# Kernel tuning notes

Hardware: AMD Instinct MI355X
Metric: run time of the kernel (lower is better)

## Reference

```python
import jax, jax.numpy as jnp
import numpy as np

B, H, T_STEPS = 256, 1024, 128


def setup_inputs() -> dict:
    key = jax.random.key(0)
    ks = jax.random.split(key, 17)
    s = 1.0 / np.sqrt(H)
    def W(k):
        return jax.random.uniform(k, (H, H), jnp.float32, -s, s)
    def b(k):
        return jax.random.uniform(k, (H,), jnp.float32, -s, s)
    names = ["Wif", "Wii", "Wio", "Wic", "Whf", "Whi", "Who", "Whc"]
    d = {}
    for i, n in enumerate(names):
        d[n] = W(ks[i])
        d["b" + n[1:]] = b(ks[8 + i])
    d["x_0"] = jax.random.normal(ks[16], (B, H), jnp.float32)
    d["T"] = T_STEPS
    return d


def reference(Wif, bif, Wii, bii, Wio, bio, Wic, bic,
              Whf, bhf, Whi, bhi, Who, bho, Whc, bhc, x_0, T):
    def step(carry, _):
        x, h, c = carry
        gf = jax.nn.sigmoid(h @ Whf.T + bhf + x @ Wif.T + bif)
        gi = jax.nn.sigmoid(h @ Whi.T + bhi + x @ Wii.T + bii)
        cp = jnp.tanh(h @ Whc.T + bhc + x @ Wic.T + bic)
        c = gf * c + gi * cp
        go = jax.nn.sigmoid(h @ Who.T + bho + x @ Wio.T + bio)
        h = go * jnp.tanh(c)
        return (h, h, c), h  # next x_input is hidden

    h0 = jnp.zeros((B, H), x_0.dtype)
    c0 = jnp.zeros((B, H), x_0.dtype)
    _, hs = jax.lax.scan(step, (x_0, h0, c0), None, length=T - 1)
    # trajectory[0] = x_0, trajectory[t+1] = hidden after step t  -> [T, B, H]
    return jnp.concatenate([x_0[None], hs], axis=0)
```

## Files before the change

### kernel.cpp

```cpp
#include <hip/hip_runtime.h>
#include <stdint.h>


#define BATCH 256
#define HID   1024

typedef __bf16 bf16_t;
typedef bf16_t bf16x8 __attribute__((ext_vector_type(8)));
typedef float  f32x16 __attribute__((ext_vector_type(16)));
typedef float  f32x4  __attribute__((ext_vector_type(4)));
typedef float  f32x2  __attribute__((ext_vector_type(2)));
typedef unsigned int u32;
typedef unsigned long long u64;

#define WC_OFF    (64ull << 20)
#define BIAS_OFF  (72ull << 20)
#define FLAG_OFF  ((72ull << 20) + (1ull << 16))

#define LDS_BYTES 131584

__device__ __forceinline__ void gload_lds16(const void* g, void* l) {
  auto gp = reinterpret_cast<const __attribute__((address_space(1))) unsigned int*>(
      reinterpret_cast<uintptr_t>(g));
  auto lp = reinterpret_cast<__attribute__((address_space(3))) unsigned int*>(
      reinterpret_cast<uintptr_t>(l));
  __builtin_amdgcn_global_load_lds(gp, lp, 16, 0, 0);
}

__global__ __launch_bounds__(256) void k_setup(
    const float* __restrict__ wf, const float* __restrict__ wi_,
    const float* __restrict__ wo, const float* __restrict__ wc,
    const float* __restrict__ hf, const float* __restrict__ hi,
    const float* __restrict__ ho, const float* __restrict__ hc,
    const float* __restrict__ bf_, const float* __restrict__ bi_,
    const float* __restrict__ bo_, const float* __restrict__ bc_,
    const float* __restrict__ hbf, const float* __restrict__ hbi,
    const float* __restrict__ hbo, const float* __restrict__ hbc,
    const float* __restrict__ x0, float* __restrict__ out,
    bf16_t* __restrict__ Wc, bf16_t* __restrict__ Wi, float* __restrict__ bias,
    bf16_t* __restrict__ hsh, u32* __restrict__ flags, int nflags)
{
  int bid = blockIdx.x;
  if (bid < 4096) {
    int r = bid, j = r >> 2, g = r & 3;
    const float *wip, *whp, *bip, *bhp;
    switch (g) {
      case 0:  wip = wf;  whp = hf; bip = bf_; bhp = hbf; break;
      case 1:  wip = wi_; whp = hi; bip = bi_; bhp = hbi; break;
      case 2:  wip = wo;  whp = ho; bip = bo_; bhp = hbo; break;
      default: wip = wc;  whp = hc; bip = bc_; bhp = hbc; break;
    }
    int k = threadIdx.x * 4;
    f32x4 a = *(const f32x4*)(wip + (size_t)j * HID + k);
    f32x4 b = *(const f32x4*)(whp + (size_t)j * HID + k);
    union { bf16_t h[4]; u64 v; } pc, pi;
#pragma unroll
    for (int t = 0; t < 4; ++t) { pc.h[t] = (bf16_t)(a[t] + b[t]); pi.h[t] = (bf16_t)a[t]; }
    *(u64*)(Wc + (size_t)r * HID + k) = pc.v;
    *(u64*)(Wi + (size_t)r * HID + k) = pi.v;
    if (threadIdx.x == 0) bias[r] = bip[j] + bhp[j];
  } else {
    int gid = (bid - 4096) * 256 + threadIdx.x;
    int i = gid * 4;
    f32x4 v = *(const f32x4*)(x0 + i);
    __builtin_nontemporal_store(v, (f32x4*)(out + i));
    union { bf16_t h[4]; u64 u; } p;
#pragma unroll
    for (int t = 0; t < 4; ++t) p.h[t] = (bf16_t)v[t];
    *(u64*)(hsh + i) = p.u;
    if (gid < nflags) flags[gid] = 0;
  }
}

__global__ __launch_bounds__(512, 2) void k_lstm(
    const bf16_t* __restrict__ Wc, const bf16_t* __restrict__ Wi,
    const float* __restrict__ bias, bf16_t* __restrict__ hsh,
    u32* __restrict__ flags, float* __restrict__ out, int T)
{
  extern __shared__ char lds[];
  char*  plds = lds + 65536;
  float* blds = (float*)(lds + 131072);

  const int tid  = threadIdx.x;
  const int bid  = blockIdx.x;
  const int mt   = bid & 7;
  const int jt   = bid >> 3;
  const int lane = tid & 63;
  const int wv   = tid >> 6;
  const int wn   = wv & 1;
  const int ks   = wv >> 1;
  const int al   = lane & 31, kh = lane >> 5;
  const int row0 = jt << 7;

  if (tid < 128) blds[tid] = bias[row0 + tid];

  const int eb   = tid >> 4;
  const int jp   = (tid & 15) << 1;
  const int bswz = (eb & 7) << 4;
  const size_t eoff_base = ((size_t)((mt << 5) + eb) << 10) + (jt << 5) + jp;
  float cst0 = 0.f, cst1 = 0.f;

  const int aswz = (al & 15) << 4;
  const int kb0  = (ks << 9) + (kh << 4);
  bf16x8 breg0[16], breg1[16];

  for (int s = 1; s < T; ++s) {
    if (s >= 2 && wv == 0) {
      const u32* f = flags + ((size_t)(s - 1) << 8) + (mt << 5);
      u32 v = (lane < 32)
          ? __hip_atomic_load(f + lane, __ATOMIC_RELAXED, __HIP_MEMORY_SCOPE_AGENT)
          : 8u;
      int guard = 0;
      while (__any(v != 8u) && guard < (1 << 20)) {
        __builtin_amdgcn_s_sleep(1);
        if (lane < 32 && v != 8u)
          v = __hip_atomic_load(f + lane, __ATOMIC_RELAXED, __HIP_MEMORY_SCOPE_AGENT);
        ++guard;
      }
    }
    __syncthreads();

    {
      const char* hp = (const char*)hsh + ((size_t)(s - 1) << 19) + ((size_t)mt << 16);
#pragma unroll
      for (int c = 0; c < 8; ++c) {
        int d = (c << 13) + (tid << 4);
        int row = d >> 11, off = d & 2047;
        gload_lds16(hp + row * 2048 + (off ^ ((row & 15) << 4)), lds + d);
      }
    }
    if (s <= 2) {
      const bf16_t* WB  = (s == 1) ? Wi : Wc;
      const bf16_t* wb0 = WB + ((size_t)(row0 + (wn << 6) + al) << 10) + (ks << 8) + (kh << 3);
      const bf16_t* wb1 = wb0 + (32 << 10);
#pragma unroll
      for (int kk = 0; kk < 16; ++kk) {
        breg0[kk] = *(const bf16x8*)(wb0 + (kk << 4));
        breg1[kk] = *(const bf16x8*)(wb1 + (kk << 4));
      }
    }
    asm volatile("s_waitcnt vmcnt(0)" ::: "memory");
    __syncthreads();

    f32x16 acc0 = {}, acc1 = {};
    {
      const char* abase = lds + al * 2048;
#pragma unroll
      for (int kk = 0; kk < 16; ++kk) {
        bf16x8 a = *(const bf16x8*)(abase + ((kb0 + (kk << 5)) ^ aswz));
        acc0 = __builtin_amdgcn_mfma_f32_32x32x16_bf16(a, breg0[kk], acc0, 0, 0, 0);
        acc1 = __builtin_amdgcn_mfma_f32_32x32x16_bf16(a, breg1[kk], acc1, 0, 0, 0);
      }
    }

#pragma unroll
    for (int r = 0; r < 16; ++r) {
      int prow = (r & 3) + ((r >> 2) << 3) + (kh << 2);
      char* pb = plds + (ks << 14) + prow * 512;
      int sw = (prow & 7) << 4;
      *(float*)(pb + ((((wn << 6) + al) << 2) ^ sw))      = acc0[r];
      *(float*)(pb + ((((wn << 6) + 32 + al) << 2) ^ sw)) = acc1[r];
    }
    __syncthreads();

    float hv[2];
#pragma unroll
    for (int e = 0; e < 2; ++e) {
      int cb = (jp + e) << 4;
      int co = cb ^ bswz;
      const char* pb = plds + eb * 512;
      f32x4 p = *(const f32x4*)(pb + co);
      p += *(const f32x4*)(pb + 16384 + co);
      p += *(const f32x4*)(pb + 32768 + co);
      p += *(const f32x4*)(pb + 49152 + co);
      f32x4 bb = *(const f32x4*)((const char*)blds + cb);
      float xf = p[0] + bb[0], xi = p[1] + bb[1], xo = p[2] + bb[2], xc = p[3] + bb[3];
      float gf = 1.f / (1.f + __expf(-xf));
      float gi = 1.f / (1.f + __expf(-xi));
      float go = 1.f / (1.f + __expf(-xo));
      float cp = tanhf(xc);
      float &cs = e ? cst1 : cst0;
      cs = gf * cs + gi * cp;
      hv[e] = go * tanhf(cs);
    }

    union { bf16_t h2[2]; u32 u; } pk;
    pk.h2[0] = (bf16_t)hv[0]; pk.h2[1] = (bf16_t)hv[1];
    __hip_atomic_store((u32*)(hsh + ((size_t)s << 18) + eoff_base), pk.u,
                       __ATOMIC_RELAXED, __HIP_MEMORY_SCOPE_AGENT);
    asm volatile("s_waitcnt vmcnt(0)" ::: "memory");
    if (lane == 0)
      __hip_atomic_fetch_add(flags + ((size_t)s << 8) + (mt << 5) + jt, 1u,
                             __ATOMIC_RELAXED, __HIP_MEMORY_SCOPE_AGENT);
    asm volatile("" ::: "memory");
    f32x2 ov; ov[0] = hv[0]; ov[1] = hv[1];
    __builtin_nontemporal_store(ov, (f32x2*)(out + ((size_t)s << 18) + eoff_base));
  }
}

extern "C" void kernel_launch(void* const* d_in, const int* in_sizes, int n_in,
                              void* d_out, int out_size, void* d_ws, size_t ws_size,
                              hipStream_t stream) {
  const float* Wif = (const float*)d_in[0];
  const float* bif = (const float*)d_in[1];
  const float* Wii = (const float*)d_in[2];
  const float* bii = (const float*)d_in[3];
  const float* Wio = (const float*)d_in[4];
  const float* bio = (const float*)d_in[5];
  const float* Wic = (const float*)d_in[6];
  const float* bic = (const float*)d_in[7];
  const float* Whf = (const float*)d_in[8];
  const float* bhf = (const float*)d_in[9];
  const float* Whi = (const float*)d_in[10];
  const float* bhi = (const float*)d_in[11];
  const float* Who = (const float*)d_in[12];
  const float* bho = (const float*)d_in[13];
  const float* Whc = (const float*)d_in[14];
  const float* bhc = (const float*)d_in[15];
  const float* x0  = (const float*)d_in[16];
  const int T = out_size / (BATCH * HID);

  char* ws = (char*)d_ws;
  bf16_t* hsh  = (bf16_t*)ws;
  bf16_t* WcP  = (bf16_t*)(ws + WC_OFF);
  bf16_t* WiP  = hsh + ((size_t)(T - 16) << 18);
  float*  bias = (float*)(ws + BIAS_OFF);
  u32*    flg  = (u32*)(ws + FLAG_OFF);
  float*  out  = (float*)d_out;

  hipFuncSetAttribute((const void*)k_lstm,
                      hipFuncAttributeMaxDynamicSharedMemorySize, LDS_BYTES);

  k_setup<<<4352, 256, 0, stream>>>(Wif, Wii, Wio, Wic, Whf, Whi, Who, Whc,
                                    bif, bii, bio, bic, bhf, bhi, bho, bhc,
                                    x0, out, WcP, WiP, bias, hsh, flg, T * 256);
  k_lstm<<<256, 512, LDS_BYTES, stream>>>(WcP, WiP, bias, hsh, flg, out, T);
}
```

Baseline: 884.1 us.

## Map batch tiles to XCC ids so each tile's workgroups share an L2

Each workgroup reads its hardware XCC id and takes a ticket from a per-XCC counter, then derives its batch tile (mt) from the XCC and its hidden-column tile (jt) from the ticket. All workgroups exchanging a batch tile's hidden state therefore sit on one XCC and share that L2, so the per-step flag polling and h handoff should stay local instead of crossing dies. The per-wave atomic flag increments are replaced by a block barrier followed by a single flag store per workgroup, and the hidden-state and output stores become plain stores instead of atomic and nontemporal ones. This assumes exactly 32 workgroups land on each of 8 XCCs; if the scheduler distributes them unevenly, tickets wrap modulo 32 and tiles collide.

```diff
diff --git a/kernel.cpp b/kernel.cpp
--- a/kernel.cpp
+++ b/kernel.cpp
@@ -17,7 +17,7 @@
 #define BIAS_OFF  (72ull << 20)
 #define FLAG_OFF  ((72ull << 20) + (1ull << 16))
 
-#define LDS_BYTES 131584
+#define LDS_BYTES 131648
 
 __device__ __forceinline__ void gload_lds16(const void* g, void* l) {
   auto gp = reinterpret_cast<const __attribute__((address_space(1))) unsigned int*>(
@@ -75,16 +75,28 @@
 __global__ __launch_bounds__(512, 2) void k_lstm(
     const bf16_t* __restrict__ Wc, const bf16_t* __restrict__ Wi,
     const float* __restrict__ bias, bf16_t* __restrict__ hsh,
-    u32* __restrict__ flags, float* __restrict__ out, int T)
+    u32* __restrict__ flags, u32* __restrict__ tick,
+    float* __restrict__ out, int T)
 {
   extern __shared__ char lds[];
-  char*  plds = lds + 65536;
-  float* blds = (float*)(lds + 131072);
+  char*  plds   = lds + 65536;
+  float* blds   = (float*)(lds + 131072);
+  u32*   wginfo = (u32*)(lds + 131584);
 
   const int tid  = threadIdx.x;
-  const int bid  = blockIdx.x;
-  const int mt   = bid & 7;
-  const int jt   = bid >> 3;
+  if (tid == 0) {
+    u32 x;
+    asm volatile("s_getreg_b32 %0, hwreg(HW_REG_XCC_ID)" : "=s"(x));
+    x &= 7;
+    u32 t = __hip_atomic_fetch_add(tick + x, 1u, __ATOMIC_RELAXED,
+                                   __HIP_MEMORY_SCOPE_AGENT);
+    wginfo[0] = x;
+    wginfo[1] = t & 31;
+  }
+  __syncthreads();
+  const int mt = wginfo[0];
+  const int jt = wginfo[1];
+
   const int lane = tid & 63;
   const int wv   = tid >> 6;
   const int wn   = wv & 1;
@@ -109,11 +121,11 @@
       const u32* f = flags + ((size_t)(s - 1) << 8) + (mt << 5);
       u32 v = (lane < 32)
           ? __hip_atomic_load(f + lane, __ATOMIC_RELAXED, __HIP_MEMORY_SCOPE_AGENT)
-          : 8u;
+          : 1u;
       int guard = 0;
-      while (__any(v != 8u) && guard < (1 << 20)) {
+      while (!__all(v != 0) && guard < (1 << 20)) {
         __builtin_amdgcn_s_sleep(1);
-        if (lane < 32 && v != 8u)
+        if (lane < 32 && v == 0)
           v = __hip_atomic_load(f + lane, __ATOMIC_RELAXED, __HIP_MEMORY_SCOPE_AGENT);
         ++guard;
       }
@@ -186,15 +198,15 @@
 
     union { bf16_t h2[2]; u32 u; } pk;
     pk.h2[0] = (bf16_t)hv[0]; pk.h2[1] = (bf16_t)hv[1];
-    __hip_atomic_store((u32*)(hsh + ((size_t)s << 18) + eoff_base), pk.u,
-                       __ATOMIC_RELAXED, __HIP_MEMORY_SCOPE_AGENT);
+    *(u32*)(hsh + ((size_t)s << 18) + eoff_base) = pk.u;
     asm volatile("s_waitcnt vmcnt(0)" ::: "memory");
-    if (lane == 0)
-      __hip_atomic_fetch_add(flags + ((size_t)s << 8) + (mt << 5) + jt, 1u,
-                             __ATOMIC_RELAXED, __HIP_MEMORY_SCOPE_AGENT);
+    __syncthreads();
+    if (tid == 0)
+      __hip_atomic_store(flags + ((size_t)s << 8) + (mt << 5) + jt, 1u,
+                         __ATOMIC_RELAXED, __HIP_MEMORY_SCOPE_AGENT);
     asm volatile("" ::: "memory");
     f32x2 ov; ov[0] = hv[0]; ov[1] = hv[1];
-    __builtin_nontemporal_store(ov, (f32x2*)(out + ((size_t)s << 18) + eoff_base));
+    *(f32x2*)(out + ((size_t)s << 18) + eoff_base) = ov;
   }
 }
 
@@ -226,6 +238,7 @@
   bf16_t* WiP  = hsh + ((size_t)(T - 16) << 18);
   float*  bias = (float*)(ws + BIAS_OFF);
   u32*    flg  = (u32*)(ws + FLAG_OFF);
+  u32*    tick = flg + ((size_t)T << 8);
   float*  out  = (float*)d_out;
 
   hipFuncSetAttribute((const void*)k_lstm,
@@ -233,6 +246,7 @@
 
   k_setup<<<4352, 256, 0, stream>>>(Wif, Wii, Wio, Wic, Whf, Whi, Who, Whc,
                                     bif, bii, bio, bic, bhf, bhi, bho, bhc,
-                                    x0, out, WcP, WiP, bias, hsh, flg, T * 256);
-  k_lstm<<<256, 512, LDS_BYTES, stream>>>(WcP, WiP, bias, hsh, flg, out, T);
-}
+                                    x0, out, WcP, WiP, bias, hsh, flg,
+                                    T * 256 + 8);
+  k_lstm<<<256, 512, LDS_BYTES, stream>>>(WcP, WiP, bias, hsh, flg, tick, out, T);
+}
```

Measured after the change: 774.2 us. 1.14x faster.
